# Kernel optimization log

Hardware: AMD Instinct MI355X
Metric: run time of the kernel (lower is better)

The kernel has to match this reference:

```python
import jax, jax.numpy as jnp
import numpy as np

HIDDEN, HEADS, HEAD_DIM = 1024, 16, 64
BSZ, SEQ = 2, 2048
SCALE = HEAD_DIM ** (-0.5)
CAUSAL = True


def setup_inputs() -> dict:
    key = jax.random.key(0)
    ks = jax.random.split(key, 7)
    inner = HEADS * HEAD_DIM
    init = lambda k, shape: jax.random.normal(k, shape, dtype=jnp.float32) * (shape[0] ** -0.5)
    return {
        "query": jax.random.normal(ks[0], (BSZ, SEQ, HIDDEN), dtype=jnp.float32),
        "key": jax.random.normal(ks[1], (BSZ, SEQ, HIDDEN), dtype=jnp.float32),
        "value": jax.random.normal(ks[2], (BSZ, SEQ, HIDDEN), dtype=jnp.float32),
        "w_q": init(ks[3], (HIDDEN, inner)),  # stored [in, out]
        "w_k": init(ks[4], (HIDDEN, inner)),
        "w_v": init(ks[5], (HIDDEN, inner)),
        "w_o": init(ks[6], (inner, HIDDEN)),
    }


def reference(query, key, value, w_q, w_k, w_v, w_o):
    bsz, q_len, _ = query.shape
    k_len = key.shape[1]

    def split_heads(x):  # [b, s, h*d] -> [b, h, s, d]
        return x.reshape(x.shape[0], x.shape[1], HEADS, HEAD_DIM).transpose(0, 2, 1, 3)

    q = split_heads(query @ w_q)
    k = split_heads(key @ w_k)
    v = split_heads(value @ w_v)

    scores = jnp.einsum("bhqd,bhkd->bhqk", q, k) * SCALE
    if CAUSAL:
        q_pos = jnp.arange(q_len)
        k_pos = jnp.arange(k_len)
        mask = (k_pos[None, :] <= q_pos[:, None]).astype(scores.dtype)
        scores = scores + (1.0 - mask)[None, None, :, :] * -10000.0
    weights = jax.nn.softmax(scores, axis=-1)
    out = jnp.einsum("bhqk,bhkd->bhqd", weights, v)
    out = out.transpose(0, 2, 1, 3).reshape(bsz, q_len, HEADS * HEAD_DIM)
    return out @ w_o
```

## Files before the change

kernel.cpp:

```cpp
#include <hip/hip_runtime.h>


using u16 = unsigned short;
typedef __bf16 bf16x8 __attribute__((ext_vector_type(8)));
typedef short  s16x8  __attribute__((ext_vector_type(8)));
typedef float  f32x4  __attribute__((ext_vector_type(4)));

#define SEQ   2048
#define QSC   0.18033688f

__device__ __forceinline__ u16 to_bf16(float f) {
  return __builtin_bit_cast(u16, (__bf16)f);
}
__device__ __forceinline__ float from_bf16(u16 v) {
  return __builtin_bit_cast(float, ((unsigned)v) << 16);
}
__device__ __forceinline__ bf16x8 frag_cast(s16x8 v) {
  return __builtin_bit_cast(bf16x8, v);
}
__device__ __forceinline__ f32x4 mfma16(bf16x8 a, bf16x8 b, f32x4 c) {
  return __builtin_amdgcn_mfma_f32_16x16x32_bf16(a, b, c, 0, 0, 0);
}
__device__ __forceinline__ void gload_lds16(const void* g, void* l) {
  __builtin_amdgcn_global_load_lds(
      (const __attribute__((address_space(1))) void*)g,
      (__attribute__((address_space(3))) void*)l, 16, 0, 0);
}

__global__ __launch_bounds__(256) void transpose_w(const float* __restrict__ wq,
                                                   const float* __restrict__ wk,
                                                   const float* __restrict__ wv,
                                                   const float* __restrict__ wo,
                                                   u16* __restrict__ wT) {
  __shared__ float tile[32][33];
  const float* src = blockIdx.z == 0 ? wq : blockIdx.z == 1 ? wk
                     : blockIdx.z == 2 ? wv : wo;
  u16* dst = wT + (size_t)blockIdx.z * 1048576;
  const int x0 = blockIdx.x * 32, y0 = blockIdx.y * 32;
  const int tx = threadIdx.x, ty = threadIdx.y;
#pragma unroll
  for (int i = 0; i < 4; ++i)
    tile[ty + i * 8][tx] = src[(size_t)(y0 + ty + i * 8) * 1024 + x0 + tx];
  __syncthreads();
#pragma unroll
  for (int i = 0; i < 4; ++i)
    dst[(size_t)(x0 + ty + i * 8) * 1024 + y0 + tx] = to_bf16(tile[tx][ty + i * 8]);
}

__global__ __launch_bounds__(256) void gemm_qkv(const float* __restrict__ Xq,
                                                const float* __restrict__ Xk,
                                                const float* __restrict__ Xv,
                                                const u16* __restrict__ WT,
                                                u16* __restrict__ Qb,
                                                u16* __restrict__ Kb,
                                                u16* __restrict__ VTb) {
  __shared__ u16 As[128 * 32];
  __shared__ u16 Bs[128 * 32];
  const int z = blockIdx.z;
  const u16* Gbf;
  const float* Gf32;
  int row0, n0;
  if (z == 2) {
    Gbf = WT + 2097152;
    Gf32 = Xv;
    row0 = blockIdx.y * 128;
    n0 = blockIdx.x * 128;
  } else {
    Gf32 = z ? Xk : Xq;
    Gbf = WT + (size_t)z * 1048576;
    row0 = blockIdx.x * 128;
    n0 = blockIdx.y * 128;
  }
  const int tid = threadIdx.x;
  const int w = tid >> 6, lane = tid & 63;
  const int g = lane >> 4, c = lane & 15;
  const int wr = w >> 1, wc = w & 1;

  f32x4 acc[4][4];
#pragma unroll
  for (int i = 0; i < 4; ++i)
#pragma unroll
    for (int j = 0; j < 4; ++j) acc[i][j] = (f32x4){0.f, 0.f, 0.f, 0.f};

  const int sub = lane >> 2;
  const int kq = lane & 3;
  const int ksrc = (kq ^ ((sub >> 1) & 3)) * 8;
  const int fsw = ((c >> 1) & 3);

  for (int kt = 0; kt < 32; ++kt) {
    const int k0 = kt * 32;
    s16x8 sreg[2];
#pragma unroll
    for (int it = 0; it < 2; ++it) {
      const int ch = w * 2 + it;
      const int row = ch * 16 + sub;
      if (z == 2) {
        gload_lds16(Gbf + (size_t)(row0 + row) * 1024 + k0 + ksrc, (char*)As + ch * 1024);
        const float4* p = (const float4*)(Gf32 + (size_t)(n0 + row) * 1024 + k0 + ksrc);
        const float4 aa = p[0], bb = p[1];
        s16x8 o;
        o[0] = (short)to_bf16(aa.x); o[1] = (short)to_bf16(aa.y);
        o[2] = (short)to_bf16(aa.z); o[3] = (short)to_bf16(aa.w);
        o[4] = (short)to_bf16(bb.x); o[5] = (short)to_bf16(bb.y);
        o[6] = (short)to_bf16(bb.z); o[7] = (short)to_bf16(bb.w);
        sreg[it] = o;
      } else {
        gload_lds16(Gbf + (size_t)(n0 + row) * 1024 + k0 + ksrc, (char*)Bs + ch * 1024);
        const float4* p = (const float4*)(Gf32 + (size_t)(row0 + row) * 1024 + k0 + ksrc);
        const float4 aa = p[0], bb = p[1];
        s16x8 o;
        o[0] = (short)to_bf16(aa.x); o[1] = (short)to_bf16(aa.y);
        o[2] = (short)to_bf16(aa.z); o[3] = (short)to_bf16(aa.w);
        o[4] = (short)to_bf16(bb.x); o[5] = (short)to_bf16(bb.y);
        o[6] = (short)to_bf16(bb.z); o[7] = (short)to_bf16(bb.w);
        sreg[it] = o;
      }
    }
    {
      char* dstbase = (z == 2) ? (char*)Bs : (char*)As;
#pragma unroll
      for (int it = 0; it < 2; ++it)
        *(s16x8*)(dstbase + (w * 2 + it) * 1024 + lane * 16) = sreg[it];
    }
    __syncthreads();

    bf16x8 af[4], bfr[4];
#pragma unroll
    for (int mi = 0; mi < 4; ++mi)
      af[mi] = frag_cast(*(const s16x8*)((const char*)As + (wr * 64 + mi * 16 + c) * 64 + ((g ^ fsw) << 4)));
#pragma unroll
    for (int ni = 0; ni < 4; ++ni)
      bfr[ni] = frag_cast(*(const s16x8*)((const char*)Bs + (wc * 64 + ni * 16 + c) * 64 + ((g ^ fsw) << 4)));
#pragma unroll
    for (int mi = 0; mi < 4; ++mi)
#pragma unroll
      for (int ni = 0; ni < 4; ++ni)
        acc[mi][ni] = mfma16(af[mi], bfr[ni], acc[mi][ni]);
    __syncthreads();
  }

  const float sc = (z == 0) ? QSC : 1.0f;
#pragma unroll
  for (int mi = 0; mi < 4; ++mi) {
    const int rowb = row0 + wr * 64 + mi * 16 + g * 4;
#pragma unroll
    for (int ni = 0; ni < 4; ++ni) {
      const int col = n0 + wc * 64 + ni * 16 + c;
#pragma unroll
      for (int r = 0; r < 4; ++r) {
        const int row = rowb + r;
        const float v = acc[mi][ni][r] * sc;
        if (z == 2) {
          const int hh = row >> 6, d = row & 63;
          const int bb = col >> 11, s = col & 2047;
          VTb[((size_t)((bb * 16 + hh) * 64 + d)) * 2048 + s] = to_bf16(v);
        } else {
          u16* C = z == 0 ? Qb : Kb;
          C[(size_t)row * 1024 + col] = to_bf16(v);
        }
      }
    }
  }
}

__global__ __launch_bounds__(256) void gemm_out(const u16* __restrict__ A,
                                                const u16* __restrict__ BT,
                                                float* __restrict__ C) {
  __shared__ u16 As[64 * 32];
  __shared__ u16 Bs[128 * 32];
  const int tid = threadIdx.x;
  const int w = tid >> 6, lane = tid & 63;
  const int g = lane >> 4, c = lane & 15;
  const int wr = w >> 1, wc = w & 1;
  const int row0 = blockIdx.x * 64;
  const int n0 = blockIdx.y * 128;

  f32x4 acc[2][4];
#pragma unroll
  for (int i = 0; i < 2; ++i)
#pragma unroll
    for (int j = 0; j < 4; ++j) acc[i][j] = (f32x4){0.f, 0.f, 0.f, 0.f};

  const int sub = lane >> 2;
  const int kq = lane & 3;
  const int ksrc = (kq ^ ((sub >> 1) & 3)) * 8;
  const int fsw = ((c >> 1) & 3);

  for (int kt = 0; kt < 32; ++kt) {
    const int k0 = kt * 32;
    {
      const int row = w * 16 + sub;
      gload_lds16(A + (size_t)(row0 + row) * 1024 + k0 + ksrc, (char*)As + w * 1024);
    }
#pragma unroll
    for (int it = 0; it < 2; ++it) {
      const int ch = w * 2 + it;
      const int row = ch * 16 + sub;
      gload_lds16(BT + (size_t)(n0 + row) * 1024 + k0 + ksrc, (char*)Bs + ch * 1024);
    }
    __syncthreads();

    bf16x8 af[2], bfr[4];
#pragma unroll
    for (int mi = 0; mi < 2; ++mi)
      af[mi] = frag_cast(*(const s16x8*)((const char*)As + (wr * 32 + mi * 16 + c) * 64 + ((g ^ fsw) << 4)));
#pragma unroll
    for (int ni = 0; ni < 4; ++ni)
      bfr[ni] = frag_cast(*(const s16x8*)((const char*)Bs + (wc * 64 + ni * 16 + c) * 64 + ((g ^ fsw) << 4)));
#pragma unroll
    for (int mi = 0; mi < 2; ++mi)
#pragma unroll
      for (int ni = 0; ni < 4; ++ni)
        acc[mi][ni] = mfma16(af[mi], bfr[ni], acc[mi][ni]);
    __syncthreads();
  }

#pragma unroll
  for (int mi = 0; mi < 2; ++mi) {
    const int rowb = row0 + wr * 32 + mi * 16 + g * 4;
#pragma unroll
    for (int ni = 0; ni < 4; ++ni) {
      const int col = n0 + wc * 64 + ni * 16 + c;
#pragma unroll
      for (int r = 0; r < 4; ++r)
        C[(size_t)(rowb + r) * 1024 + col] = acc[mi][ni][r];
    }
  }
}

__global__ __launch_bounds__(512, 4) void attn_fwd(const u16* __restrict__ Qb,
                                                   const u16* __restrict__ Kb,
                                                   const u16* __restrict__ VTb,
                                                   u16* __restrict__ PO,
                                                   float* __restrict__ ML) {
  __shared__ u16 Ks[2][128 * 64];
  __shared__ u16 VTs[2][64 * 128];

  const int tid = threadIdx.x;
  const int w = tid >> 6, lane = tid & 63;
  const int g = lane >> 4, c = lane & 15;

  const int flat = blockIdx.x + 40 * blockIdx.y;
  const int logical = (flat & 7) * 160 + (flat >> 3);
  const int slice_id = logical % 40;
  const int bh = logical / 40;
  const int b = bh >> 4, h = bh & 15;

  int sid = slice_id, x = 0;
  for (; x < 16; ++x) {
    const int ns_ = (x + 4) >> 2;
    if (sid < ns_) break;
    sid -= ns_;
  }
  const int ns = (x + 4) >> 2;
  const int np = x + 1;
  const int t0 = (sid * np) / ns, t1 = ((sid + 1) * np) / ns;
  const int sg = slice_id + 40 * bh;
  const int q0w = x * 128 + w * 16;

  bf16x8 qfr[2];
#pragma unroll
  for (int ch = 0; ch < 2; ++ch)
    qfr[ch] = frag_cast(*(const s16x8*)(Qb + (size_t)(b * SEQ + q0w + c) * 1024 + h * 64 + ch * 32 + g * 8));

  s16x8 ones_s;
#pragma unroll
  for (int j = 0; j < 8; ++j) ones_s[j] = (short)0x3F80;
  const bf16x8 onesf = frag_cast(ones_s);

  f32x4 oacc[4];
#pragma unroll
  for (int j = 0; j < 4; ++j) oacc[j] = (f32x4){0.f, 0.f, 0.f, 0.f};
  f32x4 lacc = (f32x4){0.f, 0.f, 0.f, 0.f};
  float m_run = -1e30f;

  const int srow = tid >> 3;
  const int scol = (tid & 7) * 8;
  const int vd = tid >> 4;
  const int vcol = (tid & 15) * 8;

  s16x8 kreg[2], vreg[2];
#define LOADKV(T)                                                                              \
  {                                                                                            \
    const int kv0_ = (T)*128;                                                                  \
    _Pragma("unroll") for (int it = 0; it < 2; ++it) {                                         \
      kreg[it] = *(const s16x8*)(Kb + (size_t)(b * SEQ + kv0_ + srow + it * 64) * 1024 +       \
                                 h * 64 + scol);                                               \
      vreg[it] = *(const s16x8*)(VTb + ((size_t)(bh * 64 + vd + it * 32)) * 2048 + kv0_ +      \
                                 vcol);                                                        \
    }                                                                                          \
  }
#define WRITEKV(BUF)                                                                           \
  {                                                                                            \
    _Pragma("unroll") for (int it = 0; it < 2; ++it) {                                         \
      const int rr_ = srow + it * 64;                                                          \
      const int pr_ = (rr_ & 0x63) | ((rr_ & 4) << 2) | ((rr_ & 0x18) >> 1);                   \
      *(s16x8*)((char*)Ks[BUF] + pr_ * 128 + ((scol * 2) ^ ((pr_ & 7) << 4))) = kreg[it];      \
      const int vr_ = vd + it * 32;                                                            \
      *(s16x8*)((char*)VTs[BUF] + vr_ * 256 + ((vcol * 2) ^ ((vr_ & 7) << 4))) = vreg[it];     \
    }                                                                                          \
  }

  LOADKV(t0);
  WRITEKV(0);
  __syncthreads();

  int cur = 0;
  for (int t = t0; t < t1; ++t) {
    const bool pre = (t + 1 < t1);
    if (pre) LOADKV(t + 1);

    const int kv0 = t * 128;
    if (!(kv0 > q0w + 15)) {
      f32x4 sa[8];
#pragma unroll
      for (int i = 0; i < 8; ++i) sa[i] = (f32x4){0.f, 0.f, 0.f, 0.f};
#pragma unroll
      for (int kvf = 0; kvf < 8; ++kvf) {
        const int kr = kvf * 16 + c;
        const int rb = kr * 128, swz = (kr & 7) << 4;
#pragma unroll
        for (int ch = 0; ch < 2; ++ch) {
          const bf16x8 ak = frag_cast(*(const s16x8*)((char*)Ks[cur] + rb + ((ch * 64 + g * 16) ^ swz)));
          sa[kvf] = mfma16(ak, qfr[ch], sa[kvf]);
        }
      }

      float mt = -1e30f;
      if (kv0 + 127 > q0w) {
        const int q_abs = q0w + c;
#pragma unroll
        for (int kvf = 0; kvf < 8; ++kvf) {
          const int kvb = kv0 + (kvf >> 1) * 32 + (kvf & 1) * 4 + 8 * g;
#pragma unroll
          for (int r = 0; r < 4; ++r) {
            float s = sa[kvf][r];
            if (kvb + r > q_abs) s = -30000.f;
            sa[kvf][r] = s;
            mt = fmaxf(mt, s);
          }
        }
      } else {
#pragma unroll
        for (int kvf = 0; kvf < 8; ++kvf)
#pragma unroll
          for (int r = 0; r < 4; ++r) mt = fmaxf(mt, sa[kvf][r]);
      }
      mt = fmaxf(mt, __shfl_xor(mt, 16));
      mt = fmaxf(mt, __shfl_xor(mt, 32));

      if (__any(mt > m_run + 8.f)) {
        const float m_new = fmaxf(m_run, mt);
        const float alpha = __builtin_amdgcn_exp2f(m_run - m_new);
        m_run = m_new;
#pragma unroll
        for (int r = 0; r < 4; ++r) {
          const float ar = __shfl(alpha, g * 4 + r);
#pragma unroll
          for (int df = 0; df < 4; ++df) oacc[df][r] *= ar;
          lacc[r] *= ar;
        }
      }

      s16x8 pk[4];
#pragma unroll
      for (int kvf = 0; kvf < 8; ++kvf)
#pragma unroll
        for (int r = 0; r < 4; ++r) {
          const float p = __builtin_amdgcn_exp2f(sa[kvf][r] - m_run);
          pk[kvf >> 1][(kvf & 1) * 4 + r] = (short)to_bf16(p);
        }

#pragma unroll
      for (int ch = 0; ch < 4; ++ch) {
        const bf16x8 ap = frag_cast(pk[ch]);
#pragma unroll
        for (int df = 0; df < 4; ++df) {
          const int dr = df * 16 + c;
          const bf16x8 bv = frag_cast(*(const s16x8*)((char*)VTs[cur] + dr * 256 +
                                                      ((ch * 64 + g * 16) ^ ((dr & 7) << 4))));
          oacc[df] = mfma16(ap, bv, oacc[df]);
        }
        lacc = mfma16(ap, onesf, lacc);
      }
    }

    if (pre) WRITEKV(cur ^ 1);
    __syncthreads();
    cur ^= 1;
  }

  const size_t pob = (size_t)sg * 8192;
#pragma unroll
  for (int r = 0; r < 4; ++r) {
    const int row = w * 16 + g * 4 + r;
#pragma unroll
    for (int df = 0; df < 4; ++df)
      PO[pob + row * 64 + df * 16 + c] = to_bf16(oacc[df][r]);
  }
  if (g == 0)
    ML[sg * 256 + (w * 16 + c) * 2 + 0] = m_run;
  if (c == 0) {
#pragma unroll
    for (int r = 0; r < 4; ++r)
      ML[sg * 256 + (w * 16 + g * 4 + r) * 2 + 1] = lacc[r];
  }
}

__global__ __launch_bounds__(512) void attn_merge(const u16* __restrict__ PO,
                                                  const float* __restrict__ ML,
                                                  u16* __restrict__ Ob) {
  const int x = blockIdx.x, bh = blockIdx.y;
  const int b = bh >> 4, h = bh & 15;
  const int tid = threadIdx.x;
  const int row = tid >> 2, c0 = (tid & 3) << 4;

  int base = 0;
  for (int xp = 0; xp < x; ++xp) base += (xp + 4) >> 2;
  const int ns = (x + 4) >> 2;
  const int sg0 = base + 40 * bh;

  float m[4], l[4], a[4];
  float M = -3e38f;
  for (int i = 0; i < ns; ++i) {
    m[i] = ML[(sg0 + i) * 256 + row * 2 + 0];
    l[i] = ML[(sg0 + i) * 256 + row * 2 + 1];
    M = fmaxf(M, m[i]);
  }
  float denom = 0.f;
  for (int i = 0; i < ns; ++i) {
    a[i] = __builtin_amdgcn_exp2f(m[i] - M);
    denom += a[i] * l[i];
  }
  const float inv = 1.f / denom;

  float o[16];
#pragma unroll
  for (int j = 0; j < 16; ++j) o[j] = 0.f;
  for (int i = 0; i < ns; ++i) {
    const float s = a[i] * inv;
    const u16* p = PO + (size_t)(sg0 + i) * 8192 + row * 64 + c0;
    const s16x8 v0 = *(const s16x8*)p;
    const s16x8 v1 = *(const s16x8*)(p + 8);
#pragma unroll
    for (int j = 0; j < 8; ++j) {
      o[j] += s * from_bf16((u16)v0[j]);
      o[8 + j] += s * from_bf16((u16)v1[j]);
    }
  }

  s16x8 lo, hi;
#pragma unroll
  for (int j = 0; j < 8; ++j) {
    lo[j] = (short)to_bf16(o[j]);
    hi[j] = (short)to_bf16(o[8 + j]);
  }
  u16* dst = Ob + (size_t)(b * SEQ + x * 128 + row) * 1024 + h * 64 + c0;
  *(s16x8*)dst = lo;
  *(s16x8*)(dst + 8) = hi;
}

extern "C" void kernel_launch(void* const* d_in, const int* in_sizes, int n_in,
                              void* d_out, int out_size, void* d_ws, size_t ws_size,
                              hipStream_t stream) {
  const float* query = (const float*)d_in[0];
  const float* key_ = (const float*)d_in[1];
  const float* value = (const float*)d_in[2];
  const float* w_q = (const float*)d_in[3];
  const float* w_k = (const float*)d_in[4];
  const float* w_v = (const float*)d_in[5];
  const float* w_o = (const float*)d_in[6];

  char* ws = (char*)d_ws;
  u16* PO = (u16*)(ws + 0);
  u16* wT = (u16*)(ws + 25165824);
  float* ML = (float*)(ws + 25165824);
  u16* Qb = (u16*)(ws + 33554432);
  u16* Kb = (u16*)(ws + 41943040);
  u16* VTb = (u16*)(ws + 50331648);
  u16* Ob = (u16*)(ws + 58720256);

  transpose_w<<<dim3(32, 32, 4), dim3(32, 8), 0, stream>>>(w_q, w_k, w_v, w_o, wT);
  gemm_qkv<<<dim3(32, 8, 3), 256, 0, stream>>>(query, key_, value, wT, Qb, Kb, VTb);
  attn_fwd<<<dim3(40, 32), 512, 0, stream>>>(Qb, Kb, VTb, PO, ML);
  attn_merge<<<dim3(16, 32), 512, 0, stream>>>(PO, ML, Ob);
  gemm_out<<<dim3(64, 8), 256, 0, stream>>>(Ob, wT + 3145728, (float*)d_out);
}
```

Baseline: 111.4 us.

## Double-buffer LDS tiles in QKV projection GEMM to overlap loads with MFMA

Gives the QKV projection GEMM two LDS buffers per operand. The next k-tile's fp32 activations are prefetched into registers and the bf16 weights are loaded asynchronously into the alternate buffer while MFMAs run on the current one. This drops one barrier per iteration and hides global-load latency behind compute. In exchange it doubles LDS use (32KB per block), which may lower occupancy, and adds register pressure from the prefetched float4s.

```diff
diff --git a/kernel.cpp b/kernel.cpp
--- a/kernel.cpp
+++ b/kernel.cpp
@@ -54,8 +54,8 @@
                                                 u16* __restrict__ Qb,
                                                 u16* __restrict__ Kb,
                                                 u16* __restrict__ VTb) {
-  __shared__ u16 As[128 * 32];
-  __shared__ u16 Bs[128 * 32];
+  __shared__ u16 As[2][128 * 32];
+  __shared__ u16 Bs[2][128 * 32];
   const int z = blockIdx.z;
   const u16* Gbf;
   const float* Gf32;
@@ -71,6 +71,9 @@
     row0 = blockIdx.x * 128;
     n0 = blockIdx.y * 128;
   }
+  const int frow0 = (z == 2) ? n0 : row0;
+  const int wrow0 = (z == 2) ? row0 : n0;
+
   const int tid = threadIdx.x;
   const int w = tid >> 6, lane = tid & 63;
   const int g = lane >> 4, c = lane & 15;
@@ -87,56 +90,69 @@
   const int ksrc = (kq ^ ((sub >> 1) & 3)) * 8;
   const int fsw = ((c >> 1) & 3);
 
+  float4 fa[2][2];
+#define LOADF(KT)                                                                              \
+  {                                                                                            \
+    const int k0_ = (KT)*32;                                                                   \
+    _Pragma("unroll") for (int it = 0; it < 2; ++it) {                                         \
+      const int row = (w * 2 + it) * 16 + sub;                                                 \
+      const float4* p = (const float4*)(Gf32 + (size_t)(frow0 + row) * 1024 + k0_ + ksrc);     \
+      fa[it][0] = p[0];                                                                        \
+      fa[it][1] = p[1];                                                                        \
+    }                                                                                          \
+  }
+#define GLOADW(KT, BUF)                                                                        \
+  {                                                                                            \
+    const int k0_ = (KT)*32;                                                                   \
+    char* wdst = (z == 2) ? (char*)As[BUF] : (char*)Bs[BUF];                                   \
+    _Pragma("unroll") for (int it = 0; it < 2; ++it) {                                         \
+      const int ch = w * 2 + it;                                                               \
+      const int row = ch * 16 + sub;                                                           \
+      gload_lds16(Gbf + (size_t)(wrow0 + row) * 1024 + k0_ + ksrc, wdst + ch * 1024);          \
+    }                                                                                          \
+  }
+#define WRITEF(BUF)                                                                            \
+  {                                                                                            \
+    char* fdst = (z == 2) ? (char*)Bs[BUF] : (char*)As[BUF];                                   \
+    _Pragma("unroll") for (int it = 0; it < 2; ++it) {                                         \
+      s16x8 o;                                                                                 \
+      o[0] = (short)to_bf16(fa[it][0].x); o[1] = (short)to_bf16(fa[it][0].y);                  \
+      o[2] = (short)to_bf16(fa[it][0].z); o[3] = (short)to_bf16(fa[it][0].w);                  \
+      o[4] = (short)to_bf16(fa[it][1].x); o[5] = (short)to_bf16(fa[it][1].y);                  \
+      o[6] = (short)to_bf16(fa[it][1].z); o[7] = (short)to_bf16(fa[it][1].w);                  \
+      *(s16x8*)(fdst + (w * 2 + it) * 1024 + lane * 16) = o;                                   \
+    }                                                                                          \
+  }
+
+  LOADF(0);
+  GLOADW(0, 0);
+  WRITEF(0);
+  __syncthreads();
+
+  int cur = 0;
   for (int kt = 0; kt < 32; ++kt) {
-    const int k0 = kt * 32;
-    s16x8 sreg[2];
-#pragma unroll
-    for (int it = 0; it < 2; ++it) {
-      const int ch = w * 2 + it;
-      const int row = ch * 16 + sub;
-      if (z == 2) {
-        gload_lds16(Gbf + (size_t)(row0 + row) * 1024 + k0 + ksrc, (char*)As + ch * 1024);
-        const float4* p = (const float4*)(Gf32 + (size_t)(n0 + row) * 1024 + k0 + ksrc);
-        const float4 aa = p[0], bb = p[1];
-        s16x8 o;
-        o[0] = (short)to_bf16(aa.x); o[1] = (short)to_bf16(aa.y);
-        o[2] = (short)to_bf16(aa.z); o[3] = (short)to_bf16(aa.w);
-        o[4] = (short)to_bf16(bb.x); o[5] = (short)to_bf16(bb.y);
-        o[6] = (short)to_bf16(bb.z); o[7] = (short)to_bf16(bb.w);
-        sreg[it] = o;
-      } else {
-        gload_lds16(Gbf + (size_t)(n0 + row) * 1024 + k0 + ksrc, (char*)Bs + ch * 1024);
-        const float4* p = (const float4*)(Gf32 + (size_t)(row0 + row) * 1024 + k0 + ksrc);
-        const float4 aa = p[0], bb = p[1];
-        s16x8 o;
-        o[0] = (short)to_bf16(aa.x); o[1] = (short)to_bf16(aa.y);
-        o[2] = (short)to_bf16(aa.z); o[3] = (short)to_bf16(aa.w);
-        o[4] = (short)to_bf16(bb.x); o[5] = (short)to_bf16(bb.y);
-        o[6] = (short)to_bf16(bb.z); o[7] = (short)to_bf16(bb.w);
-        sreg[it] = o;
-      }
-    }
-    {
-      char* dstbase = (z == 2) ? (char*)Bs : (char*)As;
-#pragma unroll
-      for (int it = 0; it < 2; ++it)
-        *(s16x8*)(dstbase + (w * 2 + it) * 1024 + lane * 16) = sreg[it];
-    }
-    __syncthreads();
+    const bool pre = (kt + 1 < 32);
+    if (pre) {
+      LOADF(kt + 1);
+      GLOADW(kt + 1, cur ^ 1);
+    }
 
     bf16x8 af[4], bfr[4];
 #pragma unroll
     for (int mi = 0; mi < 4; ++mi)
-      af[mi] = frag_cast(*(const s16x8*)((const char*)As + (wr * 64 + mi * 16 + c) * 64 + ((g ^ fsw) << 4)));
+      af[mi] = frag_cast(*(const s16x8*)((const char*)As[cur] + (wr * 64 + mi * 16 + c) * 64 + ((g ^ fsw) << 4)));
 #pragma unroll
     for (int ni = 0; ni < 4; ++ni)
-      bfr[ni] = frag_cast(*(const s16x8*)((const char*)Bs + (wc * 64 + ni * 16 + c) * 64 + ((g ^ fsw) << 4)));
+      bfr[ni] = frag_cast(*(const s16x8*)((const char*)Bs[cur] + (wc * 64 + ni * 16 + c) * 64 + ((g ^ fsw) << 4)));
 #pragma unroll
     for (int mi = 0; mi < 4; ++mi)
 #pragma unroll
       for (int ni = 0; ni < 4; ++ni)
         acc[mi][ni] = mfma16(af[mi], bfr[ni], acc[mi][ni]);
+
+    if (pre) WRITEF(cur ^ 1);
     __syncthreads();
+    cur ^= 1;
   }
 
   const float sc = (z == 0) ? QSC : 1.0f;
```

After: 113.6 us. No clear change (+2.0%).

## Split K across two wave groups in QKV GEMM with LDS reduction

Applied to the files above, without the earlier changes.

The QKV projection GEMM now launches 512 threads per block. Two groups of four waves each handle half of the K dimension with their own LDS tiles, and the partial accumulators are then summed through LDS before the epilogue. This doubles the waves available per output tile, so the latency of the fp32 loads and the bf16 conversion is better hidden. In exchange it adds a reduction phase with extra barriers, doubles LDS use per block, and may limit occupancy through register pressure.

```diff
diff --git a/kernel.cpp b/kernel.cpp
--- a/kernel.cpp
+++ b/kernel.cpp
@@ -47,15 +47,14 @@
     dst[(size_t)(x0 + ty + i * 8) * 1024 + y0 + tx] = to_bf16(tile[tx][ty + i * 8]);
 }
 
-__global__ __launch_bounds__(256) void gemm_qkv(const float* __restrict__ Xq,
+__global__ __launch_bounds__(512) void gemm_qkv(const float* __restrict__ Xq,
                                                 const float* __restrict__ Xk,
                                                 const float* __restrict__ Xv,
                                                 const u16* __restrict__ WT,
                                                 u16* __restrict__ Qb,
                                                 u16* __restrict__ Kb,
                                                 u16* __restrict__ VTb) {
-  __shared__ u16 As[128 * 32];
-  __shared__ u16 Bs[128 * 32];
+  __shared__ __align__(16) char lds[32768];
   const int z = blockIdx.z;
   const u16* Gbf;
   const float* Gf32;
@@ -71,10 +70,19 @@
     row0 = blockIdx.x * 128;
     n0 = blockIdx.y * 128;
   }
+  const int frow0 = (z == 2) ? n0 : row0;
+  const int wrow0 = (z == 2) ? row0 : n0;
+
   const int tid = threadIdx.x;
   const int w = tid >> 6, lane = tid & 63;
+  const int quad = w >> 2, wq = w & 3;
   const int g = lane >> 4, c = lane & 15;
-  const int wr = w >> 1, wc = w & 1;
+  const int wr = wq >> 1, wc = wq & 1;
+
+  char* As = lds + quad * 8192;
+  char* Bs = lds + 16384 + quad * 8192;
+  char* fdst = (z == 2) ? Bs : As;
+  char* wdst = (z == 2) ? As : Bs;
 
   f32x4 acc[4][4];
 #pragma unroll
@@ -86,51 +94,37 @@
   const int kq = lane & 3;
   const int ksrc = (kq ^ ((sub >> 1) & 3)) * 8;
   const int fsw = ((c >> 1) & 3);
-
-  for (int kt = 0; kt < 32; ++kt) {
-    const int k0 = kt * 32;
+  const int kbase = quad * 512;
+
+  for (int kt = 0; kt < 16; ++kt) {
+    const int k0 = kbase + kt * 32;
     s16x8 sreg[2];
 #pragma unroll
     for (int it = 0; it < 2; ++it) {
-      const int ch = w * 2 + it;
+      const int ch = wq * 2 + it;
       const int row = ch * 16 + sub;
-      if (z == 2) {
-        gload_lds16(Gbf + (size_t)(row0 + row) * 1024 + k0 + ksrc, (char*)As + ch * 1024);
-        const float4* p = (const float4*)(Gf32 + (size_t)(n0 + row) * 1024 + k0 + ksrc);
-        const float4 aa = p[0], bb = p[1];
-        s16x8 o;
-        o[0] = (short)to_bf16(aa.x); o[1] = (short)to_bf16(aa.y);
-        o[2] = (short)to_bf16(aa.z); o[3] = (short)to_bf16(aa.w);
-        o[4] = (short)to_bf16(bb.x); o[5] = (short)to_bf16(bb.y);
-        o[6] = (short)to_bf16(bb.z); o[7] = (short)to_bf16(bb.w);
-        sreg[it] = o;
-      } else {
-        gload_lds16(Gbf + (size_t)(n0 + row) * 1024 + k0 + ksrc, (char*)Bs + ch * 1024);
-        const float4* p = (const float4*)(Gf32 + (size_t)(row0 + row) * 1024 + k0 + ksrc);
-        const float4 aa = p[0], bb = p[1];
-        s16x8 o;
-        o[0] = (short)to_bf16(aa.x); o[1] = (short)to_bf16(aa.y);
-        o[2] = (short)to_bf16(aa.z); o[3] = (short)to_bf16(aa.w);
-        o[4] = (short)to_bf16(bb.x); o[5] = (short)to_bf16(bb.y);
-        o[6] = (short)to_bf16(bb.z); o[7] = (short)to_bf16(bb.w);
-        sreg[it] = o;
-      }
-    }
-    {
-      char* dstbase = (z == 2) ? (char*)Bs : (char*)As;
-#pragma unroll
-      for (int it = 0; it < 2; ++it)
-        *(s16x8*)(dstbase + (w * 2 + it) * 1024 + lane * 16) = sreg[it];
-    }
+      gload_lds16(Gbf + (size_t)(wrow0 + row) * 1024 + k0 + ksrc, wdst + ch * 1024);
+      const float4* p = (const float4*)(Gf32 + (size_t)(frow0 + row) * 1024 + k0 + ksrc);
+      const float4 aa = p[0], bb = p[1];
+      s16x8 o;
+      o[0] = (short)to_bf16(aa.x); o[1] = (short)to_bf16(aa.y);
+      o[2] = (short)to_bf16(aa.z); o[3] = (short)to_bf16(aa.w);
+      o[4] = (short)to_bf16(bb.x); o[5] = (short)to_bf16(bb.y);
+      o[6] = (short)to_bf16(bb.z); o[7] = (short)to_bf16(bb.w);
+      sreg[it] = o;
+    }
+#pragma unroll
+    for (int it = 0; it < 2; ++it)
+      *(s16x8*)(fdst + (wq * 2 + it) * 1024 + lane * 16) = sreg[it];
     __syncthreads();
 
     bf16x8 af[4], bfr[4];
 #pragma unroll
     for (int mi = 0; mi < 4; ++mi)
-      af[mi] = frag_cast(*(const s16x8*)((const char*)As + (wr * 64 + mi * 16 + c) * 64 + ((g ^ fsw) << 4)));
+      af[mi] = frag_cast(*(const s16x8*)(As + (wr * 64 + mi * 16 + c) * 64 + ((g ^ fsw) << 4)));
 #pragma unroll
     for (int ni = 0; ni < 4; ++ni)
-      bfr[ni] = frag_cast(*(const s16x8*)((const char*)Bs + (wc * 64 + ni * 16 + c) * 64 + ((g ^ fsw) << 4)));
+      bfr[ni] = frag_cast(*(const s16x8*)(Bs + (wc * 64 + ni * 16 + c) * 64 + ((g ^ fsw) << 4)));
 #pragma unroll
     for (int mi = 0; mi < 4; ++mi)
 #pragma unroll
@@ -139,6 +133,32 @@
     __syncthreads();
   }
 
+  float* red = (float*)lds;
+#pragma unroll
+  for (int pass = 0; pass < 2; ++pass) {
+    if (quad == 1) {
+#pragma unroll
+      for (int mh = 0; mh < 2; ++mh)
+#pragma unroll
+        for (int ni = 0; ni < 4; ++ni)
+#pragma unroll
+          for (int r = 0; r < 4; ++r)
+            red[(mh * 16 + ni * 4 + r) * 256 + wq * 64 + lane] = acc[pass * 2 + mh][ni][r];
+    }
+    __syncthreads();
+    if (quad == 0) {
+#pragma unroll
+      for (int mh = 0; mh < 2; ++mh)
+#pragma unroll
+        for (int ni = 0; ni < 4; ++ni)
+#pragma unroll
+          for (int r = 0; r < 4; ++r)
+            acc[pass * 2 + mh][ni][r] += red[(mh * 16 + ni * 4 + r) * 256 + wq * 64 + lane];
+    }
+    __syncthreads();
+  }
+
+  if (quad != 0) return;
   const float sc = (z == 0) ? QSC : 1.0f;
 #pragma unroll
   for (int mi = 0; mi < 4; ++mi) {
@@ -481,7 +501,7 @@
   u16* Ob = (u16*)(ws + 58720256);
 
   transpose_w<<<dim3(32, 32, 4), dim3(32, 8), 0, stream>>>(w_q, w_k, w_v, w_o, wT);
-  gemm_qkv<<<dim3(32, 8, 3), 256, 0, stream>>>(query, key_, value, wT, Qb, Kb, VTb);
+  gemm_qkv<<<dim3(32, 8, 3), 512, 0, stream>>>(query, key_, value, wT, Qb, Kb, VTb);
   attn_fwd<<<dim3(40, 32), 512, 0, stream>>>(Qb, Kb, VTb, PO, ML);
   attn_merge<<<dim3(16, 32), 512, 0, stream>>>(PO, ML, Ob);
   gemm_out<<<dim3(64, 8), 256, 0, stream>>>(Ob, wT + 3145728, (float*)d_out);
```

New measurement: 119.6 us. 1.07x slower.
